# Kernel optimization log

Measured on AMD Instinct MI355X. Metric: run time of the kernel, lower is better.

The kernel has to match this reference:

```python
import jax, jax.numpy as jnp
from jax import lax
import numpy as np

K = 2        # k-hop MIS / number of rw SpGEMM iterations
EPS = 0.5    # lazy random-walk epsilon
N = 2048     # nodes
D = 512      # feature dim
E = 65536    # edges (avg degree 32)


def setup_inputs() -> dict:
    key = jax.random.key(0)
    k1, k2, k3, k4 = jax.random.split(key, 4)
    edge_index = jax.random.randint(k1, (2, E), 0, N, dtype=jnp.int32)
    edge_attr = jax.random.uniform(k2, (E,), dtype=jnp.float32)
    x = jax.random.normal(k3, (N, D), dtype=jnp.float32)
    rank = jnp.arange(N, dtype=jnp.int32)  # node ordering ('random' ordering = some permutation; identity here)
    u = jax.random.uniform(k4, (N, N), dtype=jnp.float32)  # noise for row-wise multinomial sampling
    return {"edge_index": edge_index, "edge_attr": edge_attr, "x": x, "rank": rank, "u": u}


def _maximal_k_independent_set(row, col, rank, n, k):
    """Greedy maximal k-independent set: nodes that are local rank-minima within k hops."""
    big = jnp.int32(n)

    def prop_min(r):  # one hop of min-propagation (message row -> col), keep self
        return jnp.minimum(jax.ops.segment_min(r[row], col, num_segments=n), r)

    def prop_or(b):   # one hop of boolean OR propagation (as int32)
        return jnp.maximum(jax.ops.segment_max(b[row], col, num_segments=n), b)

    def cond(st):
        mis, mask, mr = st
        return ~jnp.all(mask)

    def body(st):
        mis, mask, mr = st
        for _ in range(k):
            mr = prop_min(mr)
        mis = mis | (rank == mr)
        mk = mis.astype(jnp.int32)
        for _ in range(k):
            mk = prop_or(mk)
        mask = mk > 0
        mr = jnp.where(mask, big, rank)
        return mis, mask, mr

    init = (jnp.zeros(n, bool), jnp.zeros(n, bool), rank)
    mis, _, _ = lax.while_loop(cond, body, init)
    return mis


def _row_normalize(m):
    s = m.sum(axis=1, keepdims=True)
    return m / jnp.where(s > 0, s, 1.0)


def reference(edge_index, edge_attr, x, rank, u):
    n = x.shape[0]
    row, col = edge_index[0], edge_index[1]

    # --- MIS over the graph structure (integer-only) ---
    mis = _maximal_k_independent_set(row, col, rank, n, K)

    # --- adjacency (dense padded form of the SparseTensor) ---
    adj = jnp.zeros((n, n), x.dtype).at[row, col].add(edge_attr)

    # --- lazy random walk: rw = D^-1 A, offdiag *= (1-eps), diag = old_diag + eps ---
    rw = _row_normalize(adj)
    di = jnp.arange(n)
    new_diag = rw[di, di] + EPS  # computed BEFORE scaling, per original code
    rw = (rw * (1.0 - EPS)).at[di, di].set(new_diag)

    # --- c_mat = rw^K @ eye[:, mis]; padded to [n, n] with zero non-MIS columns ---
    c = jnp.where(mis[None, :], jnp.eye(n, dtype=x.dtype), 0.0)
    for _ in range(K):
        c = rw @ c
    c = _row_normalize(c)

    # --- sample_partition_matrix: per-row multinomial via Gumbel-argmax ---
    g = -jnp.log(-jnp.log(u + 1e-20) + 1e-20)
    logits = jnp.where(c > 0, jnp.log(jnp.maximum(c, 1e-30)), -jnp.inf) + g
    cluster = jnp.argmax(logits, axis=1)                 # [n] cluster id (a MIS column)
    c_hard = jax.nn.one_hot(cluster, n, dtype=x.dtype)   # partition matrix [n, n]

    # --- p_inv = row-normalized c_hard.T ---
    counts = c_hard.sum(axis=0)
    p_inv = c_hard.T / jnp.where(counts > 0, counts, 1.0)[:, None]

    # --- coarsen: c^T A c, pool: p_inv @ x ---
    adj_c = c_hard.T @ adj @ c_hard
    x_pool = p_inv @ x
    return adj_c, c_hard, p_inv, mis, x_pool
```

## Files before the change

### kernel.cpp

```cpp
#include <hip/hip_runtime.h>
#include <hip/hip_bf16.h>
#include <math.h>
#include <stdint.h>

#define NN 2048
#define DD 512
#define EE 65536
#define EPSV 0.5f
#define SEN 2048
#define PADE 98304

static const size_t SZ = (size_t)NN * NN;

__global__ __launch_bounds__(256) void count_deg(const int* __restrict__ row,
                                                 const int* __restrict__ col,
                                                 int* __restrict__ degree,
                                                 int* __restrict__ cdeg) {
  int e = blockIdx.x * 256 + threadIdx.x;
  atomicAdd(&degree[row[e]], 1);
  atomicAdd(&cdeg[col[e]], 1);
}

__global__ __launch_bounds__(1024) void csr_scan_pad(const int* __restrict__ degree,
                                                     const int* __restrict__ cdeg,
                                                     int* __restrict__ row_ptr,
                                                     int* __restrict__ fill_ptr,
                                                     int* __restrict__ col_ptr,
                                                     int* __restrict__ cfill_ptr,
                                                     unsigned short* __restrict__ colidx,
                                                     unsigned short* __restrict__ rowidx,
                                                     float* __restrict__ avals,
                                                     unsigned long long* __restrict__ packed,
                                                     int* __restrict__ counts) {
  __shared__ int a[NN], b[NN], c[NN], d[NN];
  int t = threadIdx.x;
  for (int v = t; v < NN; v += 1024) {
    a[v] = (degree[v] + 15) & ~15;
    c[v] = (cdeg[v] + 15) & ~15;
    packed[v] = 0ull;
    counts[v] = 0;
  }
  __syncthreads();
  int* s1 = a; int* d1 = b; int* s2 = c; int* d2 = d;
  for (int off = 1; off < NN; off <<= 1) {
    for (int v = t; v < NN; v += 1024) {
      d1[v] = s1[v] + (v >= off ? s1[v - off] : 0);
      d2[v] = s2[v] + (v >= off ? s2[v - off] : 0);
    }
    __syncthreads();
    int* tp = s1; s1 = d1; d1 = tp;
    tp = s2; s2 = d2; d2 = tp;
  }
  for (int v = t; v < NN; v += 1024) {
    int dg = degree[v];
    int end = s1[v];
    int excl = end - ((dg + 15) & ~15);
    row_ptr[v] = excl;
    fill_ptr[v] = excl;
    for (int e = excl + dg; e < end; ++e) {
      colidx[e] = (unsigned short)v;
      avals[e] = 0.f;
    }
    dg = cdeg[v];
    end = s2[v];
    excl = end - ((dg + 15) & ~15);
    col_ptr[v] = excl;
    cfill_ptr[v] = excl;
    for (int e = excl + dg; e < end; ++e) rowidx[e] = (unsigned short)v;
  }
  if (t == 0) {
    row_ptr[NN] = s1[NN - 1];
    col_ptr[NN] = s2[NN - 1];
  }
}

__global__ __launch_bounds__(256) void csr_fill(const int* __restrict__ row,
                                                const int* __restrict__ col,
                                                const float* __restrict__ attr,
                                                int* __restrict__ fill_ptr,
                                                int* __restrict__ cfill_ptr,
                                                unsigned short* __restrict__ colidx,
                                                unsigned short* __restrict__ rowidx,
                                                float* __restrict__ avals) {
  int e = blockIdx.x * 256 + threadIdx.x;
  int r = row[e], c = col[e];
  int pos = atomicAdd(&fill_ptr[r], 1);
  colidx[pos] = (unsigned short)c;
  avals[pos] = attr[e];
  rowidx[atomicAdd(&cfill_ptr[c], 1)] = (unsigned short)r;
}

__global__ __launch_bounds__(1024) void mis_kernel(const int* __restrict__ row_ptr_g,
                                                   const int* __restrict__ col_ptr_g,
                                                   const unsigned short* __restrict__ colidx,
                                                   const unsigned short* __restrict__ rowidx,
                                                   const int* __restrict__ rank_g,
                                                   int* __restrict__ mis_flag,
                                                   int* __restrict__ mis_list,
                                                   int* __restrict__ misinv,
                                                   int* __restrict__ mis_count) {
  __shared__ int rank_s[NN];
  __shared__ int mr[NN];
  __shared__ int cov[NN];
  __shared__ int dly[NN];
  __shared__ int mis_s[NN];
  __shared__ int row_ptr_s[NN + 1];
  __shared__ int col_ptr_s[NN + 1];
  __shared__ int unc[2][NN];
  __shared__ int dl[NN];
  __shared__ int ucnt[2];
  __shared__ int dcnt;
  __shared__ int cnt;
  int t = threadIdx.x;
  const uint4* col4 = (const uint4*)colidx;
  const uint4* row4 = (const uint4*)rowidx;

  for (int v = t; v < NN; v += 1024) {
    int rk = rank_g[v];
    rank_s[v] = rk;
    mr[v] = rk;
    cov[v] = 0;
    dly[v] = 0;
    mis_s[v] = 0;
    row_ptr_s[v] = row_ptr_g[v];
    col_ptr_s[v] = col_ptr_g[v];
    unc[0][v] = v;
  }
  if (t == 0) {
    row_ptr_s[NN] = row_ptr_g[NN];
    col_ptr_s[NN] = col_ptr_g[NN];
    ucnt[0] = NN;
    ucnt[1] = 0;
    dcnt = 0;
    cnt = 0;
  }
  __syncthreads();

  int cur = 0;
  for (int round = 0; round < NN; ++round) {
    int U = ucnt[cur];
    if (round) {
      for (int v = t; v < NN; v += 1024) {
        mr[v] = cov[v] ? SEN : rank_s[v];
        dly[v] = 0;
      }
      if (t == 0) { ucnt[cur ^ 1] = 0; dcnt = 0; }
      __syncthreads();
    }
    for (int i = t; i < U; i += 1024) {
      int v = unc[cur][i];
      int val = rank_s[v];
      int e0 = row_ptr_s[v];
      int nch = (row_ptr_s[v + 1] - e0) >> 3;
      const uint4* b4 = col4 + (e0 >> 3);
      for (int cI = 0; cI < nch; cI += 2) {
        uint4 A = b4[cI], B = b4[cI + 1];
        atomicMin(&mr[A.x & 0xFFFFu], val); atomicMin(&mr[A.x >> 16], val);
        atomicMin(&mr[A.y & 0xFFFFu], val); atomicMin(&mr[A.y >> 16], val);
        atomicMin(&mr[A.z & 0xFFFFu], val); atomicMin(&mr[A.z >> 16], val);
        atomicMin(&mr[A.w & 0xFFFFu], val); atomicMin(&mr[A.w >> 16], val);
        atomicMin(&mr[B.x & 0xFFFFu], val); atomicMin(&mr[B.x >> 16], val);
        atomicMin(&mr[B.y & 0xFFFFu], val); atomicMin(&mr[B.y >> 16], val);
        atomicMin(&mr[B.z & 0xFFFFu], val); atomicMin(&mr[B.z >> 16], val);
        atomicMin(&mr[B.w & 0xFFFFu], val); atomicMin(&mr[B.w >> 16], val);
      }
    }
    __syncthreads();
    for (int i = t; i < U; i += 1024) {
      int v = unc[cur][i];
      int val = mr[v];
      int e0 = col_ptr_s[v];
      int nch = (col_ptr_s[v + 1] - e0) >> 3;
      const uint4* b4 = row4 + (e0 >> 3);
      for (int cI = 0; cI < nch; cI += 2) {
        uint4 A = b4[cI], B = b4[cI + 1];
        int m0 = min(mr[A.x & 0xFFFFu], mr[A.x >> 16]);
        int m1 = min(mr[A.y & 0xFFFFu], mr[A.y >> 16]);
        int m2 = min(mr[A.z & 0xFFFFu], mr[A.z >> 16]);
        int m3 = min(mr[A.w & 0xFFFFu], mr[A.w >> 16]);
        int m4 = min(mr[B.x & 0xFFFFu], mr[B.x >> 16]);
        int m5 = min(mr[B.y & 0xFFFFu], mr[B.y >> 16]);
        int m6 = min(mr[B.z & 0xFFFFu], mr[B.z >> 16]);
        int m7 = min(mr[B.w & 0xFFFFu], mr[B.w >> 16]);
        val = min(val, min(min(min(m0, m1), min(m2, m3)),
                           min(min(m4, m5), min(m6, m7))));
      }
      if (rank_s[v] == val) {
        mis_s[v] = 1;
        dly[v] = 1;
        dl[atomicAdd(&dcnt, 1)] = v;
      }
    }
    __syncthreads();
    int D = dcnt;
    for (int i = t; i < D; i += 1024) {
      int v = dl[i];
      int e0 = row_ptr_s[v];
      int nch = (row_ptr_s[v + 1] - e0) >> 3;
      const uint4* b4 = col4 + (e0 >> 3);
      for (int cI = 0; cI < nch; cI += 2) {
        uint4 A = b4[cI], B = b4[cI + 1];
        dly[A.x & 0xFFFFu] = 1; dly[A.x >> 16] = 1;
        dly[A.y & 0xFFFFu] = 1; dly[A.y >> 16] = 1;
        dly[A.z & 0xFFFFu] = 1; dly[A.z >> 16] = 1;
        dly[A.w & 0xFFFFu] = 1; dly[A.w >> 16] = 1;
        dly[B.x & 0xFFFFu] = 1; dly[B.x >> 16] = 1;
        dly[B.y & 0xFFFFu] = 1; dly[B.y >> 16] = 1;
        dly[B.z & 0xFFFFu] = 1; dly[B.z >> 16] = 1;
        dly[B.w & 0xFFFFu] = 1; dly[B.w >> 16] = 1;
      }
    }
    __syncthreads();
    for (int i = t; i < U; i += 1024) {
      int v = unc[cur][i];
      int c1 = dly[v];
      if (!c1) {
        int e0 = col_ptr_s[v];
        int nch = (col_ptr_s[v + 1] - e0) >> 3;
        const uint4* b4 = row4 + (e0 >> 3);
        for (int cI = 0; cI < nch; cI += 2) {
          uint4 A = b4[cI], B = b4[cI + 1];
          c1 |= dly[A.x & 0xFFFFu] | dly[A.x >> 16] |
                dly[A.y & 0xFFFFu] | dly[A.y >> 16] |
                dly[A.z & 0xFFFFu] | dly[A.z >> 16] |
                dly[A.w & 0xFFFFu] | dly[A.w >> 16] |
                dly[B.x & 0xFFFFu] | dly[B.x >> 16] |
                dly[B.y & 0xFFFFu] | dly[B.y >> 16] |
                dly[B.z & 0xFFFFu] | dly[B.z >> 16] |
                dly[B.w & 0xFFFFu] | dly[B.w >> 16];
          if (c1) break;
        }
      }
      if (c1) cov[v] = 1;
      else unc[cur ^ 1][atomicAdd(&ucnt[cur ^ 1], 1)] = v;
    }
    __syncthreads();
    if (ucnt[cur ^ 1] == 0) break;
    cur ^= 1;
  }

  for (int v = t; v < NN; v += 1024) {
    int s = mis_s[v];
    mis_flag[v] = s;
    int slot = -1;
    if (s) {
      slot = atomicAdd(&cnt, 1);
      mis_list[slot] = v;
    }
    misinv[v] = slot;
  }
  __syncthreads();
  if (t == 0) *mis_count = cnt;
}

__global__ __launch_bounds__(256) void rw_build(const int* __restrict__ row_ptr,
                                                const unsigned short* __restrict__ colidx,
                                                const float* __restrict__ avals,
                                                const int* __restrict__ misinv,
                                                float* __restrict__ rw,
                                                float* __restrict__ Bc) {
  int i = blockIdx.x;
  __shared__ float rowbuf[NN];
  __shared__ float ssum;
  int t = threadIdx.x;
  for (int j = t; j < NN; j += 256) rowbuf[j] = 0.f;
  if (t == 0) ssum = 0.f;
  __syncthreads();
  int e0 = row_ptr[i], e1 = row_ptr[i + 1];
  float part = 0.f;
  for (int e = e0 + t; e < e1; e += 256) {
    float a = avals[e];
    atomicAdd(&rowbuf[colidx[e]], a);
    part += a;
  }
  for (int off = 32; off; off >>= 1) part += __shfl_down(part, off);
  if ((t & 63) == 0) atomicAdd(&ssum, part);
  __syncthreads();
  float s = ssum;
  s = (s > 0.f) ? s : 1.f;
  for (int j = t; j < NN; j += 256) {
    float v = rowbuf[j] / s;
    v = (i == j) ? (v + EPSV) : (v * (1.f - EPSV));
    rw[(size_t)i * NN + j] = v;
    int tc = misinv[j];
    if (tc >= 0) Bc[(size_t)tc * NN + i] = v;
  }
}

__device__ inline unsigned int f32_key(float x) {
  unsigned int u = __float_as_uint(x);
  return (u & 0x80000000u) ? ~u : (u | 0x80000000u);
}
__device__ inline float dot4(float4 a, float4 b) {
  return ((a.x * b.x + a.y * b.y) + (a.z * b.z + a.w * b.w));
}
__device__ inline unsigned long long umax64(unsigned long long a, unsigned long long b) {
  return a > b ? a : b;
}
__device__ inline int pdecode(unsigned long long p) {
  return (p == 0ull) ? 0 : (NN - 1 - (int)(p & 0xFFFFFFFFull));
}

__global__ __launch_bounds__(256) void c2_argmax(const float* __restrict__ rw,
                                                 const float* __restrict__ Bc,
                                                 const float* __restrict__ u,
                                                 const int* __restrict__ mis_list,
                                                 const int* __restrict__ mis_count,
                                                 unsigned long long* __restrict__ packed) {
  int M = *mis_count;
  int ncg = (M + 3) >> 2;
  int njobs = ncg * 64;
  int lane = threadIdx.x & 63, w = threadIdx.x >> 6;
  for (int j = blockIdx.x; j < njobs; j += gridDim.x) {
    int cg = j >> 6, tile = j & 63;
    int c0 = cg * 4;
    float4 creg[4][8];
    int mcol[4];
#pragma unroll
    for (int cc = 0; cc < 4; ++cc) {
      int colv = c0 + cc;
      int cl = colv < M ? colv : (M - 1);
      mcol[cc] = mis_list[cl];
      const float4* cb = (const float4*)(Bc + (size_t)cl * NN);
#pragma unroll
      for (int q = 0; q < 8; ++q) creg[cc][q] = cb[q * 64 + lane];
    }
    int rbase = tile * 32 + w * 8;
#pragma unroll
    for (int it = 0; it < 8; ++it) {
      int r = rbase + it;
      const float4* rp = (const float4*)(rw + (size_t)r * NN);
      float4 a0 = rp[lane], a1 = rp[64 + lane], a2 = rp[128 + lane], a3 = rp[192 + lane];
      float4 a4 = rp[256 + lane], a5 = rp[320 + lane], a6 = rp[384 + lane], a7 = rp[448 + lane];
      float sacc[4];
#pragma unroll
      for (int cc = 0; cc < 4; ++cc) {
        float s01 = dot4(a0, creg[cc][0]) + dot4(a1, creg[cc][1]);
        float s23 = dot4(a2, creg[cc][2]) + dot4(a3, creg[cc][3]);
        float s45 = dot4(a4, creg[cc][4]) + dot4(a5, creg[cc][5]);
        float s67 = dot4(a6, creg[cc][6]) + dot4(a7, creg[cc][7]);
        float s = (s01 + s23) + (s45 + s67);
        s += __shfl_xor(s, 32);
        s += __shfl_xor(s, 16);
        s += __shfl_xor(s, 8);
        s += __shfl_xor(s, 4);
        s += __shfl_xor(s, 2);
        s += __shfl_xor(s, 1);
        sacc[cc] = s;
      }
      if (lane == 0) {
        unsigned long long best = 0ull;
#pragma unroll
        for (int cc = 0; cc < 4; ++cc) {
          if (c0 + cc < M && sacc[cc] > 0.f) {
            int m = mcol[cc];
            float uu = u[(size_t)r * NN + m];
            float g = -logf(-logf(uu + 1e-20f) + 1e-20f);
            float logit = logf(sacc[cc]) + g;
            unsigned long long key =
                ((unsigned long long)f32_key(logit) << 32) | (unsigned int)(NN - 1 - m);
            best = umax64(best, key);
          }
        }
        if (best) atomicMax(&packed[r], best);
      }
    }
  }
}

__global__ __launch_bounds__(256) void decode_zero(const unsigned long long* __restrict__ packed,
                                                   int* __restrict__ cluster,
                                                   int* __restrict__ counts,
                                                   float* __restrict__ adjc,
                                                   float* __restrict__ xp) {
  int idx = blockIdx.x * 256 + threadIdx.x;
  if (idx < (int)SZ) adjc[idx] = 0.f;
  else xp[idx - (int)SZ] = 0.f;
  if (idx < NN) {
    int m = pdecode(packed[idx]);
    cluster[idx] = m;
    atomicAdd(&counts[m], 1);
  }
}

__global__ __launch_bounds__(256) void scatter_chpm(const int* __restrict__ row,
                                                    const int* __restrict__ col,
                                                    const float* __restrict__ attr,
                                                    const float* __restrict__ x,
                                                    const int* __restrict__ cluster,
                                                    const int* __restrict__ counts,
                                                    const int* __restrict__ mis_flag,
                                                    float* __restrict__ out_ch,
                                                    float* __restrict__ out_pinv,
                                                    float* __restrict__ out_mis,
                                                    float* __restrict__ adjc,
                                                    float* __restrict__ xp) {
  int idx = blockIdx.x * 256 + threadIdx.x;
  int a = idx >> 11, b = idx & (NN - 1);
  out_ch[idx] = (cluster[a] == b) ? 1.f : 0.f;
  float pv = 0.f;
  if (cluster[b] == a) {
    int c = counts[a];
    pv = 1.f / (float)(c > 0 ? c : 1);
  }
  out_pinv[idx] = pv;
  if (idx < NN) out_mis[idx] = mis_flag[idx] ? 1.f : 0.f;
  if (idx < NN * DD) {
    int i = idx >> 9;
    int ci = cluster[i];
    int c = counts[ci];
    atomicAdd(&xp[ci * DD + (idx & (DD - 1))], x[idx] / (float)(c > 0 ? c : 1));
  }
  if (idx < EE) {
    atomicAdd(&adjc[(size_t)cluster[row[idx]] * NN + cluster[col[idx]]], attr[idx]);
  }
}

extern "C" void kernel_launch(void* const* d_in, const int* in_sizes, int n_in,
                              void* d_out, int out_size, void* d_ws, size_t ws_size,
                              hipStream_t stream) {
  const int*   edge_index = (const int*)d_in[0];
  const float* edge_attr  = (const float*)d_in[1];
  const float* x          = (const float*)d_in[2];
  const int*   rank       = (const int*)d_in[3];
  const float* u          = (const float*)d_in[4];
  float* out              = (float*)d_out;

  const int* row = edge_index;
  const int* col = edge_index + EE;

  float* out_adjc = out;
  float* out_ch   = out + SZ;
  float* out_pinv = out + 2 * SZ;
  float* out_mis  = out + 3 * SZ;
  float* out_xp   = out + 3 * SZ + NN;

  int*   degree    = (int*)d_ws;
  int*   cdeg      = degree + NN;
  unsigned long long* packed = (unsigned long long*)(cdeg + NN);
  int*   counts    = (int*)(packed + NN);
  int*   mis_flag  = counts + NN;
  int*   cluster   = mis_flag + NN;
  int*   mis_list  = cluster + NN;
  int*   misinv    = mis_list + NN;
  int*   mis_count = misinv + NN;
  int*   fill_ptr  = mis_count + 1;
  int*   cfill_ptr = fill_ptr + NN;
  int*   row_ptr   = cfill_ptr + NN;
  int*   col_ptr   = row_ptr + NN + 1;
  unsigned short* colidx =
      (unsigned short*)(((uintptr_t)(col_ptr + NN + 1) + 31) & ~(uintptr_t)31);
  unsigned short* rowidx = colidx + PADE;
  float* avals = (float*)(rowidx + PADE);

  hipMemsetAsync(d_ws, 0, 2 * NN * sizeof(int), stream);
  count_deg<<<EE / 256, 256, 0, stream>>>(row, col, degree, cdeg);
  csr_scan_pad<<<1, 1024, 0, stream>>>(degree, cdeg, row_ptr, fill_ptr, col_ptr,
                                       cfill_ptr, colidx, rowidx, avals, packed, counts);
  csr_fill<<<EE / 256, 256, 0, stream>>>(row, col, edge_attr, fill_ptr, cfill_ptr,
                                         colidx, rowidx, avals);
  mis_kernel<<<1, 1024, 0, stream>>>(row_ptr, col_ptr, colidx, rowidx, rank,
                                     mis_flag, mis_list, misinv, mis_count);
  rw_build<<<NN, 256, 0, stream>>>(row_ptr, colidx, avals, misinv, out_adjc, out_ch);
  c2_argmax<<<1024, 256, 0, stream>>>(out_adjc, out_ch, u, mis_list, mis_count, packed);
  decode_zero<<<(unsigned)((SZ + (size_t)NN * DD) / 256), 256, 0, stream>>>(
      packed, cluster, counts, out_adjc, out_xp);
  scatter_chpm<<<(NN * NN) / 256, 256, 0, stream>>>(row, col, edge_attr, x, cluster,
                                                    counts, mis_flag, out_ch, out_pinv,
                                                    out_mis, out_adjc, out_xp);
}
```

Before: 247.0 us.

## Use round-tagged MIS arrays to drop reset pass; gather-based x pooling

The MIS loop tags its per-round min-propagation values and delay flags with the round number, so it no longer needs a full reset pass and an extra barrier at the start of each round. Covered nodes are recorded by setting their reserved rank to a sentinel. Separately, x pooling changes from one float atomic per element of x to one block per cluster that scans all cluster ids and sums the member rows of x. This removes atomic contention on the pooled output but makes each active block loop over all nodes.

```diff
diff --git a/kernel.cpp b/kernel.cpp
--- a/kernel.cpp
+++ b/kernel.cpp
@@ -101,7 +101,7 @@
                                                    int* __restrict__ mis_count) {
   __shared__ int rank_s[NN];
   __shared__ int mr[NN];
-  __shared__ int cov[NN];
+  __shared__ int resv[NN];
   __shared__ int dly[NN];
   __shared__ int mis_s[NN];
   __shared__ int row_ptr_s[NN + 1];
@@ -118,8 +118,8 @@
   for (int v = t; v < NN; v += 1024) {
     int rk = rank_g[v];
     rank_s[v] = rk;
-    mr[v] = rk;
-    cov[v] = 0;
+    resv[v] = rk;
+    mr[v] = 0x7FFFFFFF;
     dly[v] = 0;
     mis_s[v] = 0;
     row_ptr_s[v] = row_ptr_g[v];
@@ -139,17 +139,12 @@
   int cur = 0;
   for (int round = 0; round < NN; ++round) {
     int U = ucnt[cur];
-    if (round) {
-      for (int v = t; v < NN; v += 1024) {
-        mr[v] = cov[v] ? SEN : rank_s[v];
-        dly[v] = 0;
-      }
-      if (t == 0) { ucnt[cur ^ 1] = 0; dcnt = 0; }
-      __syncthreads();
-    }
+    int mtag = NN - round;
+    int msg_base = mtag << 12;
+    int dtag = round + 1;
     for (int i = t; i < U; i += 1024) {
       int v = unc[cur][i];
-      int val = rank_s[v];
+      int val = msg_base | rank_s[v];
       int e0 = row_ptr_s[v];
       int nch = (row_ptr_s[v + 1] - e0) >> 3;
       const uint4* b4 = col4 + (e0 >> 3);
@@ -166,33 +161,36 @@
       }
     }
     __syncthreads();
+#define EFF(w) min(resv[w], ((mr[w] >> 12) == mtag) ? (mr[w] & 4095) : SEN)
     for (int i = t; i < U; i += 1024) {
       int v = unc[cur][i];
-      int val = mr[v];
+      int val = EFF(v);
       int e0 = col_ptr_s[v];
       int nch = (col_ptr_s[v + 1] - e0) >> 3;
       const uint4* b4 = row4 + (e0 >> 3);
       for (int cI = 0; cI < nch; cI += 2) {
         uint4 A = b4[cI], B = b4[cI + 1];
-        int m0 = min(mr[A.x & 0xFFFFu], mr[A.x >> 16]);
-        int m1 = min(mr[A.y & 0xFFFFu], mr[A.y >> 16]);
-        int m2 = min(mr[A.z & 0xFFFFu], mr[A.z >> 16]);
-        int m3 = min(mr[A.w & 0xFFFFu], mr[A.w >> 16]);
-        int m4 = min(mr[B.x & 0xFFFFu], mr[B.x >> 16]);
-        int m5 = min(mr[B.y & 0xFFFFu], mr[B.y >> 16]);
-        int m6 = min(mr[B.z & 0xFFFFu], mr[B.z >> 16]);
-        int m7 = min(mr[B.w & 0xFFFFu], mr[B.w >> 16]);
+        int m0 = min(EFF(A.x & 0xFFFFu), EFF(A.x >> 16));
+        int m1 = min(EFF(A.y & 0xFFFFu), EFF(A.y >> 16));
+        int m2 = min(EFF(A.z & 0xFFFFu), EFF(A.z >> 16));
+        int m3 = min(EFF(A.w & 0xFFFFu), EFF(A.w >> 16));
+        int m4 = min(EFF(B.x & 0xFFFFu), EFF(B.x >> 16));
+        int m5 = min(EFF(B.y & 0xFFFFu), EFF(B.y >> 16));
+        int m6 = min(EFF(B.z & 0xFFFFu), EFF(B.z >> 16));
+        int m7 = min(EFF(B.w & 0xFFFFu), EFF(B.w >> 16));
         val = min(val, min(min(min(m0, m1), min(m2, m3)),
                            min(min(m4, m5), min(m6, m7))));
       }
       if (rank_s[v] == val) {
         mis_s[v] = 1;
-        dly[v] = 1;
+        dly[v] = dtag;
         dl[atomicAdd(&dcnt, 1)] = v;
       }
     }
+#undef EFF
     __syncthreads();
     int D = dcnt;
+    if (t == 0) ucnt[cur ^ 1] = 0;
     for (int i = t; i < D; i += 1024) {
       int v = dl[i];
       int e0 = row_ptr_s[v];
@@ -200,40 +198,41 @@
       const uint4* b4 = col4 + (e0 >> 3);
       for (int cI = 0; cI < nch; cI += 2) {
         uint4 A = b4[cI], B = b4[cI + 1];
-        dly[A.x & 0xFFFFu] = 1; dly[A.x >> 16] = 1;
-        dly[A.y & 0xFFFFu] = 1; dly[A.y >> 16] = 1;
-        dly[A.z & 0xFFFFu] = 1; dly[A.z >> 16] = 1;
-        dly[A.w & 0xFFFFu] = 1; dly[A.w >> 16] = 1;
-        dly[B.x & 0xFFFFu] = 1; dly[B.x >> 16] = 1;
-        dly[B.y & 0xFFFFu] = 1; dly[B.y >> 16] = 1;
-        dly[B.z & 0xFFFFu] = 1; dly[B.z >> 16] = 1;
-        dly[B.w & 0xFFFFu] = 1; dly[B.w >> 16] = 1;
+        dly[A.x & 0xFFFFu] = dtag; dly[A.x >> 16] = dtag;
+        dly[A.y & 0xFFFFu] = dtag; dly[A.y >> 16] = dtag;
+        dly[A.z & 0xFFFFu] = dtag; dly[A.z >> 16] = dtag;
+        dly[A.w & 0xFFFFu] = dtag; dly[A.w >> 16] = dtag;
+        dly[B.x & 0xFFFFu] = dtag; dly[B.x >> 16] = dtag;
+        dly[B.y & 0xFFFFu] = dtag; dly[B.y >> 16] = dtag;
+        dly[B.z & 0xFFFFu] = dtag; dly[B.z >> 16] = dtag;
+        dly[B.w & 0xFFFFu] = dtag; dly[B.w >> 16] = dtag;
       }
     }
     __syncthreads();
     for (int i = t; i < U; i += 1024) {
       int v = unc[cur][i];
-      int c1 = dly[v];
+      int c1 = (dly[v] == dtag);
       if (!c1) {
         int e0 = col_ptr_s[v];
         int nch = (col_ptr_s[v + 1] - e0) >> 3;
         const uint4* b4 = row4 + (e0 >> 3);
         for (int cI = 0; cI < nch; cI += 2) {
           uint4 A = b4[cI], B = b4[cI + 1];
-          c1 |= dly[A.x & 0xFFFFu] | dly[A.x >> 16] |
-                dly[A.y & 0xFFFFu] | dly[A.y >> 16] |
-                dly[A.z & 0xFFFFu] | dly[A.z >> 16] |
-                dly[A.w & 0xFFFFu] | dly[A.w >> 16] |
-                dly[B.x & 0xFFFFu] | dly[B.x >> 16] |
-                dly[B.y & 0xFFFFu] | dly[B.y >> 16] |
-                dly[B.z & 0xFFFFu] | dly[B.z >> 16] |
-                dly[B.w & 0xFFFFu] | dly[B.w >> 16];
+          c1 |= (dly[A.x & 0xFFFFu] == dtag) | (dly[A.x >> 16] == dtag) |
+                (dly[A.y & 0xFFFFu] == dtag) | (dly[A.y >> 16] == dtag) |
+                (dly[A.z & 0xFFFFu] == dtag) | (dly[A.z >> 16] == dtag) |
+                (dly[A.w & 0xFFFFu] == dtag) | (dly[A.w >> 16] == dtag) |
+                (dly[B.x & 0xFFFFu] == dtag) | (dly[B.x >> 16] == dtag) |
+                (dly[B.y & 0xFFFFu] == dtag) | (dly[B.y >> 16] == dtag) |
+                (dly[B.z & 0xFFFFu] == dtag) | (dly[B.z >> 16] == dtag) |
+                (dly[B.w & 0xFFFFu] == dtag) | (dly[B.w >> 16] == dtag);
           if (c1) break;
         }
       }
-      if (c1) cov[v] = 1;
+      if (c1) resv[v] = SEN;
       else unc[cur ^ 1][atomicAdd(&ucnt[cur ^ 1], 1)] = v;
     }
+    if (t == 0) dcnt = 0;
     __syncthreads();
     if (ucnt[cur ^ 1] == 0) break;
     cur ^= 1;
@@ -395,6 +394,7 @@
                                                     float* __restrict__ out_mis,
                                                     float* __restrict__ adjc,
                                                     float* __restrict__ xp) {
+  __shared__ int cl_s[NN];
   int idx = blockIdx.x * 256 + threadIdx.x;
   int a = idx >> 11, b = idx & (NN - 1);
   out_ch[idx] = (cluster[a] == b) ? 1.f : 0.f;
@@ -405,14 +405,27 @@
   }
   out_pinv[idx] = pv;
   if (idx < NN) out_mis[idx] = mis_flag[idx] ? 1.f : 0.f;
-  if (idx < NN * DD) {
-    int i = idx >> 9;
-    int ci = cluster[i];
-    int c = counts[ci];
-    atomicAdd(&xp[ci * DD + (idx & (DD - 1))], x[idx] / (float)(c > 0 ? c : 1));
-  }
   if (idx < EE) {
     atomicAdd(&adjc[(size_t)cluster[row[idx]] * NN + cluster[col[idx]]], attr[idx]);
+  }
+  int j = blockIdx.x;
+  if (j < NN) {
+    int c = counts[j];
+    if (c > 0) {
+      for (int i = threadIdx.x; i < NN; i += 256) cl_s[i] = cluster[i];
+      __syncthreads();
+      float inv = 1.f / (float)c;
+      int d0 = threadIdx.x, d1 = threadIdx.x + 256;
+      float a0 = 0.f, a1 = 0.f;
+      for (int i = 0; i < NN; ++i) {
+        if (cl_s[i] == j) {
+          a0 += x[i * DD + d0];
+          a1 += x[i * DD + d1];
+        }
+      }
+      xp[j * DD + d0] = a0 * inv;
+      xp[j * DD + d1] = a1 * inv;
+    }
   }
 }
 
```

New measurement: 402.1 us. 1.63x slower.
